# Kernel tuning notes

Measured on AMD Instinct MI355X. Metric: run time of the kernel, lower is better.

The kernel has to match this reference:

```python
import jax, jax.numpy as jnp
import numpy as np

B, N, S, D1, D2 = 16, 4096, 1024, 64, 256
IN_CH, OUT_CH = D1 + D2, 256
BN_EPS = 1e-5


def setup_inputs() -> dict:
    key = jax.random.key(0)
    ks = jax.random.split(key, 5)
    xyz1 = jax.random.normal(ks[0], (B, N, 3), dtype=jnp.float32)
    xyz2 = jax.random.normal(ks[1], (B, S, 3), dtype=jnp.float32)
    points1 = jax.random.normal(ks[2], (B, D1, N), dtype=jnp.float32)
    points2 = jax.random.normal(ks[3], (B, D2, S), dtype=jnp.float32)
    # Conv1d(kernel_size=1, bias=False) weight, squeezed to [out, in]
    W = jax.random.normal(ks[4], (OUT_CH, IN_CH), dtype=jnp.float32) * 0.05
    gamma = jnp.ones((OUT_CH,), dtype=jnp.float32)
    beta = jnp.zeros((OUT_CH,), dtype=jnp.float32)
    return dict(xyz1=xyz1, xyz2=xyz2, points1=points1, points2=points2,
                W=W, gamma=gamma, beta=beta)


def reference(xyz1, xyz2, points1, points2, W, gamma, beta):
    # --- three_nn: squared pairwise distances [B, N, S] + top-3 nearest ---
    d2 = (jnp.sum(xyz1 * xyz1, axis=-1, keepdims=True)          # [B,N,1]
          + jnp.sum(xyz2 * xyz2, axis=-1)[:, None, :]            # [B,1,S]
          - 2.0 * jnp.einsum('bnd,bsd->bns', xyz1, xyz2))        # [B,N,S]
    neg_d, idx = jax.lax.top_k(-d2, 3)                           # [B,N,3]
    dists = -neg_d
    # inverse-distance weights
    dist_recip = 1.0 / (dists + 1e-8)
    weight = dist_recip / jnp.sum(dist_recip, axis=2, keepdims=True)  # [B,N,3]
    # --- three_interpolate: gather + weighted sum ---
    p2 = jnp.swapaxes(points2, 1, 2)                             # [B,S,C]
    gathered = jax.vmap(lambda p, i: p[i])(p2, idx)              # [B,N,3,C]
    interp = jnp.einsum('bnkc,bnk->bcn', gathered, weight)       # [B,C,N]
    # --- concat skip features + ConvBNReLU1D (1x1 conv, bias=False) ---
    x = jnp.concatenate([points1, interp], axis=1)               # [B,IN_CH,N]
    y = jnp.einsum('oc,bcn->bon', W, x)                          # [B,OUT_CH,N]
    # BatchNorm1d in training mode: biased batch stats over (B, N)
    mean = jnp.mean(y, axis=(0, 2), keepdims=True)
    var = jnp.mean(jnp.square(y - mean), axis=(0, 2), keepdims=True)
    y = (y - mean) * jax.lax.rsqrt(var + BN_EPS)
    y = y * gamma[None, :, None] + beta[None, :, None]
    return jax.nn.relu(y)
```

## Files before the change

kernel.cpp:

```cpp
#include <hip/hip_runtime.h>
#include <stdint.h>


#define B_   16
#define N_   4096
#define S_   1024
#define D1_  64
#define D2_  256
#define OC_  256

typedef __attribute__((ext_vector_type(8))) short bf16x8;
typedef __attribute__((ext_vector_type(4))) float f32x4;
typedef __attribute__((ext_vector_type(4))) unsigned int u32x4;
typedef __attribute__((ext_vector_type(2))) unsigned int u32x2;

#define IDXW_OFF 0u
#define ZTB_OFF  2097152u
#define Y1_OFF   10485760u
#define Y2_OFF   44040192u
#define PART_OFF 77594624u
#define W1B_OFF  77662208u
#define W2B_OFF  77694976u
#define WS_NEED  77826048u

__device__ __forceinline__ uint16_t f2bf(float f) {
    union { float f; uint32_t u; } v; v.f = f;
    uint32_t r = v.u + 0x7FFFu + ((v.u >> 16) & 1u);
    return (uint16_t)(r >> 16);
}
__device__ __forceinline__ float bf2f(uint32_t h) {
    union { uint32_t u; float f; } v; v.u = h << 16;
    return v.f;
}

#define INSERT(d, sidx, d0, d1, d2, i0, i1, i2) do {                      \
    bool ca = (d) < (d2); bool cb = (d) < (d1); bool cc = (d) < (d0);     \
    float _n1 = __builtin_amdgcn_fmed3f((d), (d0), (d1));                 \
    float _n2 = __builtin_amdgcn_fmed3f((d), (d1), (d2));                 \
    int _j2 = cb ? (i1) : (ca ? (sidx) : (i2));                           \
    int _j1 = cc ? (i0) : (cb ? (sidx) : (i1));                           \
    i0 = cc ? (sidx) : (i0);                                              \
    d0 = fminf((d), (d0)); d1 = _n1; d2 = _n2; i1 = _j1; i2 = _j2;        \
} while (0)

__global__ void __launch_bounds__(256, 8)
k01(const float* __restrict__ xyz1, const float* __restrict__ xyz2,
    int* __restrict__ idxw, const float* __restrict__ W,
    uint16_t* __restrict__ w1b, uint16_t* __restrict__ w2b) {
    __shared__ float4 pts[8 * 129];
    int i = blockIdx.x;
    int t = threadIdx.x;
    if (i >= 2048) {
        int e = (i - 2048) * 256 + t;
        if (e < OC_ * 320) {
            int o = e / 320, c = e % 320;
            uint16_t b = f2bf(W[e]);
            if (c < 64) w1b[o * 64 + c] = b;
            else        w2b[o * 256 + (c - 64)] = b;
        }
        return;
    }
    int b  = i >> 7;
    int n0 = (i & 127) * 32;

    for (int s = t; s < S_; s += 256) {
        const float* p = xyz2 + ((size_t)b * S_ + s) * 3;
        pts[(s >> 7) * 129 + (s & 127)] = make_float4(p[0], p[1], p[2], 0.f);
    }
    __syncthreads();

    int chunk = t & 7, nidx = t >> 3;
    int n = n0 + nidx;
    const float* q = xyz1 + ((size_t)b * N_ + n) * 3;
    float ax = q[0], ay = q[1], az = q[2];

    float d0 = 3.4e38f, d1 = 3.4e38f, d2 = 3.4e38f;
    int   i0 = 0, i1 = 0, i2 = 0;

    const float4* base = pts + chunk * 129;
    int sbase = chunk * 128;
    #pragma unroll 4
    for (int j = 0; j < 128; j++) {
        float4 qq = base[j];
        int s = sbase + j;
        float dx = ax - qq.x, dy = ay - qq.y, dz = az - qq.z;
        float d = fmaf(dz, dz, fmaf(dy, dy, dx * dx));
        INSERT(d, s, d0, d1, d2, i0, i1, i2);
    }
    #pragma unroll
    for (int m = 1; m <= 4; m <<= 1) {
        float e0 = __shfl_xor(d0, m), e1 = __shfl_xor(d1, m), e2 = __shfl_xor(d2, m);
        int   g0 = __shfl_xor(i0, m), g1 = __shfl_xor(i1, m), g2 = __shfl_xor(i2, m);
        INSERT(e0, g0, d0, d1, d2, i0, i1, i2);
        INSERT(e1, g1, d0, d1, d2, i0, i1, i2);
        INSERT(e2, g2, d0, d1, d2, i0, i1, i2);
    }
    if (chunk == 0) {
        float r0 = 1.0f / (d0 + 1e-8f), r1 = 1.0f / (d1 + 1e-8f), r2 = 1.0f / (d2 + 1e-8f);
        float rs = r0 + r1 + r2;
        float* fw = (float*)idxw;
        int bb = (b * N_ + n) * 8;
        idxw[bb + 0] = i0; idxw[bb + 1] = i1; idxw[bb + 2] = i2;
        fw[bb + 4] = r0 / rs; fw[bb + 5] = r1 / rs; fw[bb + 6] = r2 / rs;
    }
}

__global__ void __launch_bounds__(256, 8)
k2f(const float* __restrict__ p2, const uint16_t* __restrict__ w2b,
    uint16_t* __restrict__ ztb, const float* __restrict__ p1,
    const uint16_t* __restrict__ w1b, uint16_t* __restrict__ y1) {
    __shared__ char smem[16384];
    int i = blockIdx.x;
    int t = threadIdx.x, l = t & 63, w = t >> 6;
    if (i < 512) {
        uint16_t* a_t = (uint16_t*)smem;
        int b = i >> 5, s0 = (i & 31) * 32;
        int sA = t & 31, cpg = t >> 5;
        const float* p2b = p2 + (size_t)b * D2_ * S_ + s0;
        #pragma unroll
        for (int j = 0; j < 16; j++) {
            int cp = cpg + 8 * j;
            float lo = p2b[(size_t)(2 * cp) * S_ + sA];
            float hi = p2b[(size_t)(2 * cp + 1) * S_ + sA];
            uint32_t pk = (uint32_t)f2bf(lo) | ((uint32_t)f2bf(hi) << 16);
            *(uint32_t*)((char*)a_t + sA * 512 + ((cp * 4) ^ ((sA & 7) << 4))) = pk;
        }
        __syncthreads();
        f32x4 acc[2][4] = {};
        int ls = l & 15, swzs = (ls & 7) << 4;
        #pragma unroll
        for (int ks = 0; ks < 8; ks++) {
            int co = ks * 32 + (l >> 4) * 8;
            bf16x8 a0 = *(const bf16x8*)((const char*)a_t + ls * 512 + ((co * 2) ^ swzs));
            bf16x8 a1 = *(const bf16x8*)((const char*)a_t + (16 + ls) * 512 + ((co * 2) ^ swzs));
            bf16x8 bbf[4];
            #pragma unroll
            for (int oj = 0; oj < 4; oj++) {
                int o = w * 64 + oj * 16 + ls;
                bbf[oj] = *(const bf16x8*)(w2b + (size_t)o * 256 + co);
            }
            #pragma unroll
            for (int oj = 0; oj < 4; oj++) {
                acc[0][oj] = __builtin_amdgcn_mfma_f32_16x16x32_bf16(a0, bbf[oj], acc[0][oj], 0, 0, 0);
                acc[1][oj] = __builtin_amdgcn_mfma_f32_16x16x32_bf16(a1, bbf[oj], acc[1][oj], 0, 0, 0);
            }
        }
        #pragma unroll
        for (int mi = 0; mi < 2; mi++)
            #pragma unroll
            for (int oj = 0; oj < 4; oj++) {
                int og = w * 4 + oj;
                uint16_t* zb = ztb + ((size_t)(b * 16 + og) * S_ + s0 + mi * 16 + (l >> 4) * 4) * 16 + ls;
                #pragma unroll
                for (int r = 0; r < 4; r++)
                    zb[(size_t)r * 16] = f2bf(acc[mi][oj][r]);
            }
    } else {
        int j2 = i - 512;
        int b = j2 >> 7, n0 = (j2 & 127) * 32;
        int oW = w * 64;
        uint16_t* pt = (uint16_t*)smem;
        {
            int nn = t & 31;
            const float* p1b = p1 + (size_t)b * D1_ * N_ + n0;
            #pragma unroll
            for (int j = 0; j < 4; j++) {
                int cp = (t >> 5) + 8 * j;
                float lo = p1b[(size_t)(2 * cp) * N_ + nn];
                float hi = p1b[(size_t)(2 * cp + 1) * N_ + nn];
                uint32_t pk = (uint32_t)f2bf(lo) | ((uint32_t)f2bf(hi) << 16);
                *(uint32_t*)((char*)pt + nn * 128 + ((cp * 4) ^ ((nn & 7) << 4))) = pk;
            }
        }
        bf16x8 af[2][4];
        #pragma unroll
        for (int ks = 0; ks < 2; ks++)
            #pragma unroll
            for (int mi = 0; mi < 4; mi++) {
                int o = oW + mi * 16 + (l & 15);
                af[ks][mi] = *(const bf16x8*)(w1b + (size_t)o * 64 + ks * 32 + (l >> 4) * 8);
            }
        f32x4 acc[4][2] = {};
        __syncthreads();
        #pragma unroll
        for (int ks = 0; ks < 2; ks++) {
            bf16x8 bf[2];
            int co = ks * 32 + (l >> 4) * 8;
            #pragma unroll
            for (int bj = 0; bj < 2; bj++) {
                int nn = bj * 16 + (l & 15);
                bf[bj] = *(const bf16x8*)((const char*)pt + nn * 128 + ((co * 2) ^ ((nn & 7) << 4)));
            }
            #pragma unroll
            for (int mi = 0; mi < 4; mi++)
                #pragma unroll
                for (int bj = 0; bj < 2; bj++)
                    acc[mi][bj] = __builtin_amdgcn_mfma_f32_16x16x32_bf16(
                        af[ks][mi], bf[bj], acc[mi][bj], 0, 0, 0);
        }
        #pragma unroll
        for (int mi = 0; mi < 4; mi++) {
            int og = w * 4 + mi;
            uint16_t* yb = y1 + ((size_t)(b * 16 + og)) * N_ * 16;
            #pragma unroll
            for (int bj = 0; bj < 2; bj++) {
                int n = n0 + bj * 16 + (l & 15);
                int oo = (l >> 4) * 4;
                u32x2 v;
                v.x = (uint32_t)f2bf(acc[mi][bj][0]) | ((uint32_t)f2bf(acc[mi][bj][1]) << 16);
                v.y = (uint32_t)f2bf(acc[mi][bj][2]) | ((uint32_t)f2bf(acc[mi][bj][3]) << 16);
                __builtin_nontemporal_store(v, (u32x2*)(yb + (size_t)n * 16 + oo));
            }
        }
    }
}

__global__ void __launch_bounds__(1024, 8)
k3a(const uint16_t* __restrict__ y1, const uint16_t* __restrict__ ztb,
    const int* __restrict__ idxw, uint16_t* __restrict__ y2,
    float* __restrict__ partials) {
    __shared__ char zsm[49152];
    __shared__ float red[16][16][2];
    int bi = blockIdx.x;
    int b = bi >> 5, og = (bi >> 1) & 15, nh = bi & 1;
    int u = threadIdx.x, l = u & 63, w = u >> 6;
    {
        const u32x4* src = (const u32x4*)(ztb + ((size_t)(b * 16 + og)) * S_ * 16);
        #pragma unroll
        for (int k = 0; k < 2; k++) {
            int g = k * 1024 + u;
            u32x4 v = src[g];
            *(u32x4*)(zsm + (g >> 1) * 48 + (g & 1) * 16) = v;
        }
    }
    __syncthreads();
    int q = l >> 2, sub = l & 3;
    float s1l[4] = {0.f, 0.f, 0.f, 0.f}, s2l[4] = {0.f, 0.f, 0.f, 0.f};
    int nbase = nh * 2048 + w * 128;
    const uint16_t* y1b = y1 + ((size_t)(b * 16 + og)) * N_ * 16;
    uint16_t* y2b = y2 + ((size_t)(b * 16 + og)) * N_ * 16;
    #pragma unroll 2
    for (int it = 0; it < 8; it++) {
        int n = nbase + it * 16 + q;
        u32x2 y1v = __builtin_nontemporal_load((const u32x2*)(y1b + (size_t)n * 16 + sub * 4));
        const int* ib = idxw + ((size_t)(b * N_ + n)) * 8;
        int4   iv = *(const int4*)ib;
        float4 wv = *((const float4*)ib + 1);
        u32x2 z0 = *(const u32x2*)(zsm + iv.x * 48 + sub * 8);
        u32x2 z1 = *(const u32x2*)(zsm + iv.y * 48 + sub * 8);
        u32x2 z2 = *(const u32x2*)(zsm + iv.z * 48 + sub * 8);
        float a0 = bf2f(y1v.x & 0xffff) + wv.x * bf2f(z0.x & 0xffff) + wv.y * bf2f(z1.x & 0xffff) + wv.z * bf2f(z2.x & 0xffff);
        float a1 = bf2f(y1v.x >> 16)    + wv.x * bf2f(z0.x >> 16)    + wv.y * bf2f(z1.x >> 16)    + wv.z * bf2f(z2.x >> 16);
        float a2 = bf2f(y1v.y & 0xffff) + wv.x * bf2f(z0.y & 0xffff) + wv.y * bf2f(z1.y & 0xffff) + wv.z * bf2f(z2.y & 0xffff);
        float a3 = bf2f(y1v.y >> 16)    + wv.x * bf2f(z0.y >> 16)    + wv.y * bf2f(z1.y >> 16)    + wv.z * bf2f(z2.y >> 16);
        s1l[0] += a0; s2l[0] += a0 * a0;
        s1l[1] += a1; s2l[1] += a1 * a1;
        s1l[2] += a2; s2l[2] += a2 * a2;
        s1l[3] += a3; s2l[3] += a3 * a3;
        u32x2 vv;
        vv.x = (uint32_t)f2bf(a0) | ((uint32_t)f2bf(a1) << 16);
        vv.y = (uint32_t)f2bf(a2) | ((uint32_t)f2bf(a3) << 16);
        __builtin_nontemporal_store(vv, (u32x2*)(y2b + (size_t)n * 16 + sub * 4));
    }
    #pragma unroll
    for (int m = 4; m <= 32; m <<= 1)
        #pragma unroll
        for (int j = 0; j < 4; j++) {
            s1l[j] += __shfl_xor(s1l[j], m);
            s2l[j] += __shfl_xor(s2l[j], m);
        }
    if (l < 4) {
        #pragma unroll
        for (int j = 0; j < 4; j++) {
            red[w][sub * 4 + j][0] = s1l[j];
            red[w][sub * 4 + j][1] = s2l[j];
        }
    }
    __syncthreads();
    if (u < 32) {
        int oi = u >> 1, st = u & 1;
        float s = 0.f;
        #pragma unroll
        for (int ww = 0; ww < 16; ww++) s += red[ww][oi][st];
        partials[(size_t)bi * 32 + oi * 2 + st] = s;
    }
}

__global__ void __launch_bounds__(256, 8)
k3c(const uint16_t* __restrict__ y2, const float* __restrict__ partials,
    const float* __restrict__ gamma, const float* __restrict__ beta,
    float* __restrict__ out) {
    __shared__ uint16_t ty[16 * 256];
    __shared__ float stat[32];
    __shared__ float sbsh[32];
    int bi = blockIdx.x;
    int b = bi >> 8, og = (bi >> 4) & 15, nc = bi & 15;
    int u = threadIdx.x;
    const uint16_t* src = y2 + (((size_t)(b * 16 + og)) * N_ + nc * 256) * 16;
    u32x4 va = __builtin_nontemporal_load((const u32x4*)(src + (size_t)u * 16));
    u32x4 vb = __builtin_nontemporal_load((const u32x4*)(src + (size_t)u * 16 + 8));
    if (u < 32) {
        int oi = u >> 1, st = u & 1;
        float s = 0.f;
        #pragma unroll 4
        for (int t2 = 0; t2 < 32; t2++) {
            int row = (t2 >> 1) * 32 + og * 2 + (t2 & 1);
            s += partials[(size_t)row * 32 + oi * 2 + st];
        }
        stat[u] = s;
    }
    __syncthreads();
    if (u < 16) {
        float mean = stat[u * 2] / 65536.0f;
        float var  = stat[u * 2 + 1] / 65536.0f - mean * mean;
        int o_g = og * 16 + u;
        float scale = gamma[o_g] * rsqrtf(var + 1e-5f);
        sbsh[u * 2]     = scale;
        sbsh[u * 2 + 1] = beta[o_g] - mean * scale;
    }
    uint32_t words[8] = {va.x, va.y, va.z, va.w, vb.x, vb.y, vb.z, vb.w};
    #pragma unroll
    for (int h = 0; h < 8; h++) {
        int o0 = h * 2, o1 = h * 2 + 1;
        *(uint16_t*)((char*)ty + o0 * 512 + ((u * 2) ^ ((o0 & 7) << 4))) = (uint16_t)(words[h] & 0xffff);
        *(uint16_t*)((char*)ty + o1 * 512 + ((u * 2) ^ ((o1 & 7) << 4))) = (uint16_t)(words[h] >> 16);
    }
    __syncthreads();
    int o = u >> 4, k = u & 15;
    int x = (o & 7) << 4;
    int o_g = og * 16 + o;
    float scale = sbsh[o * 2], bias = sbsh[o * 2 + 1];
    float* dst = out + ((size_t)(b * OC_ + o_g)) * N_ + nc * 256;
    #pragma unroll
    for (int g2 = 0; g2 < 4; g2++) {
        uint64_t z = *(const uint64_t*)((const char*)ty + o * 512 + ((g2 * 128 + k * 8) ^ x));
        f32x4 r;
        r.x = fmaxf(0.f, fmaf(bf2f((uint32_t)(z       ) & 0xffff), scale, bias));
        r.y = fmaxf(0.f, fmaf(bf2f((uint32_t)(z >> 16 ) & 0xffff), scale, bias));
        r.z = fmaxf(0.f, fmaf(bf2f((uint32_t)(z >> 32 ) & 0xffff), scale, bias));
        r.w = fmaxf(0.f, fmaf(bf2f((uint32_t)(z >> 48 ) & 0xffff), scale, bias));
        __builtin_nontemporal_store(r, (f32x4*)(dst + g2 * 64 + k * 4));
    }
}

extern "C" void kernel_launch(void* const* d_in, const int* in_sizes, int n_in,
                              void* d_out, int out_size, void* d_ws, size_t ws_size,
                              hipStream_t stream) {
    const float* xyz1  = (const float*)d_in[0];
    const float* xyz2  = (const float*)d_in[1];
    const float* p1    = (const float*)d_in[2];
    const float* p2    = (const float*)d_in[3];
    const float* W     = (const float*)d_in[4];
    const float* gamma = (const float*)d_in[5];
    const float* beta  = (const float*)d_in[6];
    float* out = (float*)d_out;
    char* ws = (char*)d_ws;
    if (ws_size < (size_t)WS_NEED) return;

    int*      idxw     = (int*)(ws + IDXW_OFF);
    uint16_t* ztb      = (uint16_t*)(ws + ZTB_OFF);
    uint16_t* y1       = (uint16_t*)(ws + Y1_OFF);
    uint16_t* y2       = (uint16_t*)(ws + Y2_OFF);
    float*    partials = (float*)(ws + PART_OFF);
    uint16_t* w1b      = (uint16_t*)(ws + W1B_OFF);
    uint16_t* w2b      = (uint16_t*)(ws + W2B_OFF);

    hipLaunchKernelGGL(k01, dim3(2368), dim3(256),  0, stream,
                       xyz1, xyz2, idxw, W, w1b, w2b);
    hipLaunchKernelGGL(k2f, dim3(2560), dim3(256),  0, stream,
                       p2, w2b, ztb, p1, w1b, y1);
    hipLaunchKernelGGL(k3a, dim3(512),  dim3(1024), 0, stream,
                       y1, ztb, idxw, y2, partials);
    hipLaunchKernelGGL(k3c, dim3(4096), dim3(256),  0, stream,
                       y2, partials, gamma, beta, out);
}
```

Before: 100.5 us.

## Merge three-NN and GEMM prelaunch kernels, convert weights to bf16 on the fly

Combines the three_nn kernel and the points1/points2 projection GEMM kernel into one launch with a block-index dispatch, since neither depends on the other. The separate weight-to-bf16 conversion pass is removed: the GEMM blocks now read fp32 W directly and convert eight values at a time in registers. This saves one kernel launch and the dependency barrier between the two stages, and lets the compute-heavy three_nn blocks overlap with the GEMM blocks. In exchange, every GEMM block re-reads and re-converts fp32 weights, which doubles weight read traffic, and shared memory grows slightly to hold the larger of the two branch layouts.

```diff
diff --git a/kernel.cpp b/kernel.cpp
--- a/kernel.cpp
+++ b/kernel.cpp
@@ -19,8 +19,6 @@
 #define Y1_OFF   10485760u
 #define Y2_OFF   44040192u
 #define PART_OFF 77594624u
-#define W1B_OFF  77662208u
-#define W2B_OFF  77694976u
 #define WS_NEED  77826048u
 
 __device__ __forceinline__ uint16_t f2bf(float f) {
@@ -31,6 +29,16 @@
 __device__ __forceinline__ float bf2f(uint32_t h) {
     union { uint32_t u; float f; } v; v.u = h << 16;
     return v.f;
+}
+__device__ __forceinline__ bf16x8 cvt8(const float* p) {
+    f32x4 a = *(const f32x4*)p;
+    f32x4 b = *(const f32x4*)(p + 4);
+    union { uint32_t u[4]; bf16x8 v; } r;
+    r.u[0] = (uint32_t)f2bf(a.x) | ((uint32_t)f2bf(a.y) << 16);
+    r.u[1] = (uint32_t)f2bf(a.z) | ((uint32_t)f2bf(a.w) << 16);
+    r.u[2] = (uint32_t)f2bf(b.x) | ((uint32_t)f2bf(b.y) << 16);
+    r.u[3] = (uint32_t)f2bf(b.z) | ((uint32_t)f2bf(b.w) << 16);
+    return r.v;
 }
 
 #define INSERT(d, sidx, d0, d1, d2, i0, i1, i2) do {                      \
@@ -44,72 +52,11 @@
 } while (0)
 
 __global__ void __launch_bounds__(256, 8)
-k01(const float* __restrict__ xyz1, const float* __restrict__ xyz2,
-    int* __restrict__ idxw, const float* __restrict__ W,
-    uint16_t* __restrict__ w1b, uint16_t* __restrict__ w2b) {
-    __shared__ float4 pts[8 * 129];
-    int i = blockIdx.x;
-    int t = threadIdx.x;
-    if (i >= 2048) {
-        int e = (i - 2048) * 256 + t;
-        if (e < OC_ * 320) {
-            int o = e / 320, c = e % 320;
-            uint16_t b = f2bf(W[e]);
-            if (c < 64) w1b[o * 64 + c] = b;
-            else        w2b[o * 256 + (c - 64)] = b;
-        }
-        return;
-    }
-    int b  = i >> 7;
-    int n0 = (i & 127) * 32;
-
-    for (int s = t; s < S_; s += 256) {
-        const float* p = xyz2 + ((size_t)b * S_ + s) * 3;
-        pts[(s >> 7) * 129 + (s & 127)] = make_float4(p[0], p[1], p[2], 0.f);
-    }
-    __syncthreads();
-
-    int chunk = t & 7, nidx = t >> 3;
-    int n = n0 + nidx;
-    const float* q = xyz1 + ((size_t)b * N_ + n) * 3;
-    float ax = q[0], ay = q[1], az = q[2];
-
-    float d0 = 3.4e38f, d1 = 3.4e38f, d2 = 3.4e38f;
-    int   i0 = 0, i1 = 0, i2 = 0;
-
-    const float4* base = pts + chunk * 129;
-    int sbase = chunk * 128;
-    #pragma unroll 4
-    for (int j = 0; j < 128; j++) {
-        float4 qq = base[j];
-        int s = sbase + j;
-        float dx = ax - qq.x, dy = ay - qq.y, dz = az - qq.z;
-        float d = fmaf(dz, dz, fmaf(dy, dy, dx * dx));
-        INSERT(d, s, d0, d1, d2, i0, i1, i2);
-    }
-    #pragma unroll
-    for (int m = 1; m <= 4; m <<= 1) {
-        float e0 = __shfl_xor(d0, m), e1 = __shfl_xor(d1, m), e2 = __shfl_xor(d2, m);
-        int   g0 = __shfl_xor(i0, m), g1 = __shfl_xor(i1, m), g2 = __shfl_xor(i2, m);
-        INSERT(e0, g0, d0, d1, d2, i0, i1, i2);
-        INSERT(e1, g1, d0, d1, d2, i0, i1, i2);
-        INSERT(e2, g2, d0, d1, d2, i0, i1, i2);
-    }
-    if (chunk == 0) {
-        float r0 = 1.0f / (d0 + 1e-8f), r1 = 1.0f / (d1 + 1e-8f), r2 = 1.0f / (d2 + 1e-8f);
-        float rs = r0 + r1 + r2;
-        float* fw = (float*)idxw;
-        int bb = (b * N_ + n) * 8;
-        idxw[bb + 0] = i0; idxw[bb + 1] = i1; idxw[bb + 2] = i2;
-        fw[bb + 4] = r0 / rs; fw[bb + 5] = r1 / rs; fw[bb + 6] = r2 / rs;
-    }
-}
-
-__global__ void __launch_bounds__(256, 8)
-k2f(const float* __restrict__ p2, const uint16_t* __restrict__ w2b,
-    uint16_t* __restrict__ ztb, const float* __restrict__ p1,
-    const uint16_t* __restrict__ w1b, uint16_t* __restrict__ y1) {
-    __shared__ char smem[16384];
+kA(const float* __restrict__ xyz1, const float* __restrict__ xyz2,
+   int* __restrict__ idxw, const float* __restrict__ W,
+   const float* __restrict__ p1, const float* __restrict__ p2,
+   uint16_t* __restrict__ ztb, uint16_t* __restrict__ y1) {
+    __shared__ char smem[16512];
     int i = blockIdx.x;
     int t = threadIdx.x, l = t & 63, w = t >> 6;
     if (i < 512) {
@@ -137,7 +84,7 @@
             #pragma unroll
             for (int oj = 0; oj < 4; oj++) {
                 int o = w * 64 + oj * 16 + ls;
-                bbf[oj] = *(const bf16x8*)(w2b + (size_t)o * 256 + co);
+                bbf[oj] = cvt8(W + (size_t)o * 320 + 64 + co);
             }
             #pragma unroll
             for (int oj = 0; oj < 4; oj++) {
@@ -155,8 +102,54 @@
                 for (int r = 0; r < 4; r++)
                     zb[(size_t)r * 16] = f2bf(acc[mi][oj][r]);
             }
+    } else if (i < 2560) {
+        int j1 = i - 512;
+        int b  = j1 >> 7;
+        int n0 = (j1 & 127) * 32;
+        float4* pts = (float4*)smem;
+
+        for (int s = t; s < S_; s += 256) {
+            const float* p = xyz2 + ((size_t)b * S_ + s) * 3;
+            pts[(s >> 7) * 129 + (s & 127)] = make_float4(p[0], p[1], p[2], 0.f);
+        }
+        __syncthreads();
+
+        int chunk = t & 7, nidx = t >> 3;
+        int n = n0 + nidx;
+        const float* q = xyz1 + ((size_t)b * N_ + n) * 3;
+        float ax = q[0], ay = q[1], az = q[2];
+
+        float d0 = 3.4e38f, d1 = 3.4e38f, d2 = 3.4e38f;
+        int   i0 = 0, i1 = 0, i2 = 0;
+
+        const float4* base = pts + chunk * 129;
+        int sbase = chunk * 128;
+        #pragma unroll 4
+        for (int j = 0; j < 128; j++) {
+            float4 qq = base[j];
+            int s = sbase + j;
+            float dx = ax - qq.x, dy = ay - qq.y, dz = az - qq.z;
+            float d = fmaf(dz, dz, fmaf(dy, dy, dx * dx));
+            INSERT(d, s, d0, d1, d2, i0, i1, i2);
+        }
+        #pragma unroll
+        for (int m = 1; m <= 4; m <<= 1) {
+            float e0 = __shfl_xor(d0, m), e1 = __shfl_xor(d1, m), e2 = __shfl_xor(d2, m);
+            int   g0 = __shfl_xor(i0, m), g1 = __shfl_xor(i1, m), g2 = __shfl_xor(i2, m);
+            INSERT(e0, g0, d0, d1, d2, i0, i1, i2);
+            INSERT(e1, g1, d0, d1, d2, i0, i1, i2);
+            INSERT(e2, g2, d0, d1, d2, i0, i1, i2);
+        }
+        if (chunk == 0) {
+            float r0 = 1.0f / (d0 + 1e-8f), r1 = 1.0f / (d1 + 1e-8f), r2 = 1.0f / (d2 + 1e-8f);
+            float rs = r0 + r1 + r2;
+            float* fw = (float*)idxw;
+            int bb = (b * N_ + n) * 8;
+            idxw[bb + 0] = i0; idxw[bb + 1] = i1; idxw[bb + 2] = i2;
+            fw[bb + 4] = r0 / rs; fw[bb + 5] = r1 / rs; fw[bb + 6] = r2 / rs;
+        }
     } else {
-        int j2 = i - 512;
+        int j2 = i - 2560;
         int b = j2 >> 7, n0 = (j2 & 127) * 32;
         int oW = w * 64;
         uint16_t* pt = (uint16_t*)smem;
@@ -178,7 +171,7 @@
             #pragma unroll
             for (int mi = 0; mi < 4; mi++) {
                 int o = oW + mi * 16 + (l & 15);
-                af[ks][mi] = *(const bf16x8*)(w1b + (size_t)o * 64 + ks * 32 + (l >> 4) * 8);
+                af[ks][mi] = cvt8(W + (size_t)o * 320 + ks * 32 + (l >> 4) * 8);
             }
         f32x4 acc[4][2] = {};
         __syncthreads();
@@ -362,13 +355,9 @@
     uint16_t* y1       = (uint16_t*)(ws + Y1_OFF);
     uint16_t* y2       = (uint16_t*)(ws + Y2_OFF);
     float*    partials = (float*)(ws + PART_OFF);
-    uint16_t* w1b      = (uint16_t*)(ws + W1B_OFF);
-    uint16_t* w2b      = (uint16_t*)(ws + W2B_OFF);
-
-    hipLaunchKernelGGL(k01, dim3(2368), dim3(256),  0, stream,
-                       xyz1, xyz2, idxw, W, w1b, w2b);
-    hipLaunchKernelGGL(k2f, dim3(2560), dim3(256),  0, stream,
-                       p2, w2b, ztb, p1, w1b, y1);
+
+    hipLaunchKernelGGL(kA,  dim3(4608), dim3(256),  0, stream,
+                       xyz1, xyz2, idxw, W, p1, p2, ztb, y1);
     hipLaunchKernelGGL(k3a, dim3(512),  dim3(1024), 0, stream,
                        y1, ztb, idxw, y2, partials);
     hipLaunchKernelGGL(k3c, dim3(4096), dim3(256),  0, stream,
```

After: 97.04 us. 3.4% less time.
